# Performance work log

Measured on AMD Instinct MI355X. Metric: run time of the kernel, lower is better.

The kernel has to match this reference:

```python
import jax, jax.numpy as jnp
import numpy as np
from jax import lax

B, T, E, D, CC, K, H = 64, 2000, 512, 1024, 32, 31, 128
PAD = (K - 1) // 2


def setup_inputs() -> dict:
    key = jax.random.key(0)
    ks = jax.random.split(key, 12)
    enc_output = jax.random.normal(ks[0], (B, T, E), dtype=jnp.float32)
    text_len = jax.random.randint(ks[1], (B,), 1, T + 1)
    dec_state = jax.random.normal(ks[2], (B, D), dtype=jnp.float32)
    prev_att_w = jax.random.uniform(ks[3], (B, T), dtype=jnp.float32)
    # learned parameters
    W_enc = jax.random.normal(ks[4], (E, H), dtype=jnp.float32) / np.sqrt(E)
    b_enc = jnp.zeros((H,), dtype=jnp.float32)
    W_dec = jax.random.normal(ks[5], (D, H), dtype=jnp.float32) / np.sqrt(D)
    W_att = jax.random.normal(ks[6], (CC, H), dtype=jnp.float32) / np.sqrt(CC)
    conv_w = jax.random.normal(ks[7], (CC, 1, K), dtype=jnp.float32) / np.sqrt(K)  # OIH
    W_out = jax.random.normal(ks[8], (H, 1), dtype=jnp.float32) / np.sqrt(H)
    b_out = jnp.zeros((1,), dtype=jnp.float32)
    return {
        'enc_output': enc_output, 'text_len': text_len, 'dec_state': dec_state,
        'prev_att_w': prev_att_w, 'W_enc': W_enc, 'b_enc': b_enc, 'W_dec': W_dec,
        'W_att': W_att, 'conv_w': conv_w, 'W_out': W_out, 'b_out': b_out,
    }


def reference(enc_output, text_len, dec_state, prev_att_w,
              W_enc, b_enc, W_dec, W_att, conv_w, W_out, b_out):
    # processed_memory = fc_enc(enc_output): (B,T,H)
    pm = jnp.einsum('bte,eh->bth', enc_output, W_enc) + b_enc
    # location conv: (B,1,T) -> (B,CC,T), same padding, no bias
    att_conv = lax.conv_general_dilated(
        prev_att_w[:, None, :], conv_w, window_strides=(1,),
        padding=[(PAD, PAD)], dimension_numbers=('NCH', 'OIH', 'NCH'))
    # fc_att on channel dim: (B,T,H)
    att_conv = jnp.einsum('bct,ch->bth', att_conv, W_att)
    # fc_dec(dec_state): (B,1,H)
    dec = (dec_state @ W_dec)[:, None, :]
    # energy: (B,T)
    energy = (jnp.tanh(att_conv + pm + dec) @ W_out)[..., 0] + b_out[0]
    att_w = jax.nn.softmax(energy, axis=1)  # (B,T)
    att_c = jnp.einsum('bte,bt->be', enc_output, att_w)  # (B,E)
    return att_c, att_w
```

## Files before the change

### kernel.cpp

```cpp
#include <hip/hip_runtime.h>

typedef short bf16x8 __attribute__((ext_vector_type(8)));
typedef float f32x4 __attribute__((ext_vector_type(4)));


__device__ __forceinline__ unsigned short f2bf(float f) {
  unsigned int u = __builtin_bit_cast(unsigned int, f);
  u += 0x7fffu + ((u >> 16) & 1u);
  return (unsigned short)(u >> 16);
}

__global__ __launch_bounds__(128) void prep_dec_kernel(
    const float* __restrict__ dec_state, const float* __restrict__ W_dec,
    const float* __restrict__ b_enc, float* __restrict__ decb)
{
  const int b = blockIdx.x;
  const int h = threadIdx.x;
  __shared__ float sd[1024];
  for (int i = h; i < 1024; i += 128) sd[i] = dec_state[b*1024 + i];
  __syncthreads();
  float acc = b_enc[h];
  #pragma unroll 8
  for (int d = 0; d < 1024; ++d) acc = fmaf(sd[d], W_dec[d*128 + h], acc);
  decb[b*128 + h] = acc;
}

__global__ __launch_bounds__(256) void prep_misc_kernel(
    const float* __restrict__ conv_w, const float* __restrict__ W_att,
    const float* __restrict__ W_enc, float* __restrict__ Mkh,
    unsigned short* __restrict__ WT)
{
  if (blockIdx.x == 64) {
    const int h = threadIdx.x;
    if (h < 128) {
      for (int k = 0; k < 31; ++k) {
        float a = 0.f;
        #pragma unroll
        for (int c = 0; c < 32; ++c) a = fmaf(conv_w[c*31 + k], W_att[c*128 + h], a);
        Mkh[k*128 + h] = a;
      }
    }
  } else {
    const int e0 = blockIdx.x * 8;
    #pragma unroll
    for (int j = 0; j < 4; ++j) {
      int idx = threadIdx.x + j*256;
      int el = idx >> 7, h = idx & 127;
      int e = e0 + el;
      float v = W_enc[e*128 + h];
      WT[(e >> 6)*8192 + h*64 + (e & 63)] = f2bf(v);
    }
  }
}

__global__ __launch_bounds__(256) void energy_kernel(
    const float* __restrict__ enc, const float* __restrict__ prev,
    const unsigned short* __restrict__ WT, const float* __restrict__ Mkh,
    const float* __restrict__ decb, const float* __restrict__ W_out,
    float* __restrict__ energy)
{
  __shared__ __align__(16) unsigned short sA[64*64];
  __shared__ __align__(16) unsigned short sB[128*64];
  __shared__ float sM[31*128];
  __shared__ float sDecb[128];
  __shared__ float sWout[128];
  __shared__ float sPrev[96];

  const int b  = blockIdx.y;
  const int t0 = blockIdx.x * 64;
  const int tid = threadIdx.x;

  for (int i = tid; i < 31*128; i += 256) sM[i] = Mkh[i];
  if (tid < 128) { sDecb[tid] = decb[b*128 + tid]; sWout[tid] = W_out[tid]; }
  if (tid < 96) {
    int tt = t0 + tid - 15;
    sPrev[tid] = (tt >= 0 && tt < 2000) ? prev[b*2000 + tt] : 0.f;
  }

  f32x4 acc[8];
  #pragma unroll
  for (int i = 0; i < 8; ++i) acc[i] = (f32x4){0.f, 0.f, 0.f, 0.f};

  const int wave = tid >> 6, lane = tid & 63;
  const int lr = lane & 15, lg = lane >> 4;
  char* sAc = (char*)sA;
  char* sBc = (char*)sB;
  const int xorv = (lr & 7) << 4;
  const int rowA = (wave*16 + lr) * 128;

  const float* encB = enc + (size_t)b * (2000u*512u);
  const float* gsrc[4]; int dstA[4];
  #pragma unroll
  for (int i = 0; i < 4; ++i) {
    int s = tid + i*256;
    int tl = s >> 4, e4 = s & 15;
    int tg = t0 + tl; if (tg > 1999) tg = 1999;
    gsrc[i] = encB + (size_t)tg*512 + e4*4;
    dstA[i] = (tl*128 + e4*8) ^ ((tl & 7) << 4);
  }
  const int hB = tid >> 1, halfB = tid & 1;

  for (int kc = 0; kc < 8; ++kc) {
    #pragma unroll
    for (int i = 0; i < 4; ++i) {
      const float4 v = *reinterpret_cast<const float4*>(gsrc[i] + kc*64);
      uint2 w;
      w.x = ((unsigned)f2bf(v.y) << 16) | f2bf(v.x);
      w.y = ((unsigned)f2bf(v.w) << 16) | f2bf(v.z);
      *reinterpret_cast<uint2*>(sAc + dstA[i]) = w;
    }
    {
      const unsigned short* src = WT + kc*8192 + tid*32;
      #pragma unroll
      for (int q = 0; q < 4; ++q) {
        uint4 v = *reinterpret_cast<const uint4*>(src + q*8);
        *reinterpret_cast<uint4*>(sBc + ((hB*128 + halfB*64 + q*16) ^ ((hB & 7) << 4))) = v;
      }
    }
    __syncthreads();
    #pragma unroll
    for (int ks = 0; ks < 2; ++ks) {
      bf16x8 a = *reinterpret_cast<const bf16x8*>(sAc + ((rowA + ks*64 + lg*16) ^ xorv));
      #pragma unroll
      for (int nt = 0; nt < 8; ++nt) {
        bf16x8 bb = *reinterpret_cast<const bf16x8*>(
            sBc + (((nt*16 + lr)*128 + ks*64 + lg*16) ^ xorv));
        acc[nt] = __builtin_amdgcn_mfma_f32_16x16x32_bf16(a, bb, acc[nt], 0, 0, 0);
      }
    }
    __syncthreads();
  }

  const int tbase = wave*16 + lg*4;
  #pragma unroll 1
  for (int k = 0; k < 31; ++k) {
    float p0 = sPrev[tbase + 0 + k];
    float p1 = sPrev[tbase + 1 + k];
    float p2 = sPrev[tbase + 2 + k];
    float p3 = sPrev[tbase + 3 + k];
    const float* mrow = sM + k*128 + lr;
    #pragma unroll
    for (int nt = 0; nt < 8; ++nt) {
      float m = mrow[nt*16];
      acc[nt][0] = fmaf(p0, m, acc[nt][0]);
      acc[nt][1] = fmaf(p1, m, acc[nt][1]);
      acc[nt][2] = fmaf(p2, m, acc[nt][2]);
      acc[nt][3] = fmaf(p3, m, acc[nt][3]);
    }
  }

  float es0 = 0.f, es1 = 0.f, es2 = 0.f, es3 = 0.f;
  #pragma unroll
  for (int nt = 0; nt < 8; ++nt) {
    float dh = sDecb[nt*16 + lr];
    float wo = sWout[nt*16 + lr];
    es0 += tanhf(acc[nt][0] + dh) * wo;
    es1 += tanhf(acc[nt][1] + dh) * wo;
    es2 += tanhf(acc[nt][2] + dh) * wo;
    es3 += tanhf(acc[nt][3] + dh) * wo;
  }
  #pragma unroll
  for (int off = 1; off < 16; off <<= 1) {
    es0 += __shfl_xor(es0, off, 64);
    es1 += __shfl_xor(es1, off, 64);
    es2 += __shfl_xor(es2, off, 64);
    es3 += __shfl_xor(es3, off, 64);
  }
  if (lr == 0) {
    int t = t0 + tbase;
    float ev[4] = {es0, es1, es2, es3};
    #pragma unroll
    for (int r = 0; r < 4; ++r)
      if (t + r < 2000) energy[b*2000 + t + r] = ev[r];
  }
}

__global__ __launch_bounds__(256) void softmax_kernel(
    const float* __restrict__ energy, float* __restrict__ attw)
{
  const int b = blockIdx.x, tid = threadIdx.x;
  __shared__ float red[4];
  __shared__ float red2[4];
  float m = -1e30f;
  for (int i = tid; i < 2000; i += 256) m = fmaxf(m, energy[b*2000 + i]);
  #pragma unroll
  for (int off = 1; off < 64; off <<= 1) m = fmaxf(m, __shfl_xor(m, off, 64));
  if ((tid & 63) == 0) red[tid >> 6] = m;
  __syncthreads();
  m = fmaxf(fmaxf(red[0], red[1]), fmaxf(red[2], red[3]));

  float s = 0.f;
  for (int i = tid; i < 2000; i += 256) {
    float p = __expf(energy[b*2000 + i] - m);
    attw[b*2000 + i] = p;
    s += p;
  }
  #pragma unroll
  for (int off = 1; off < 64; off <<= 1) s += __shfl_xor(s, off, 64);
  if ((tid & 63) == 0) red2[tid >> 6] = s;
  __syncthreads();
  s = red2[0] + red2[1] + red2[2] + red2[3];
  float inv = 1.f / s;
  for (int i = tid; i < 2000; i += 256) attw[b*2000 + i] *= inv;
}

__global__ __launch_bounds__(256) void attc_partial_kernel(
    const float* __restrict__ enc, const float* __restrict__ attw,
    float* __restrict__ part)
{
  const int b = blockIdx.y, ch = blockIdx.x, tid = threadIdx.x;
  const int tstart = ch * 125, tend = tstart + 125;
  float a0 = 0.f, a1 = 0.f;
  const float2* e2 = reinterpret_cast<const float2*>(enc + (size_t)b * (2000u*512u));
  for (int t = tstart; t < tend; ++t) {
    float w = attw[b*2000 + t];
    float2 v = e2[t*256 + tid];
    a0 = fmaf(v.x, w, a0);
    a1 = fmaf(v.y, w, a1);
  }
  part[((b*16 + ch)*512) + tid*2 + 0] = a0;
  part[((b*16 + ch)*512) + tid*2 + 1] = a1;
}

__global__ __launch_bounds__(512) void attc_reduce_kernel(
    const float* __restrict__ part, float* __restrict__ out)
{
  const int b = blockIdx.x, e = threadIdx.x;
  float s = 0.f;
  #pragma unroll
  for (int c = 0; c < 16; ++c) s += part[(b*16 + c)*512 + e];
  out[b*512 + e] = s;
}

extern "C" void kernel_launch(void* const* d_in, const int* in_sizes, int n_in,
                              void* d_out, int out_size, void* d_ws, size_t ws_size,
                              hipStream_t stream) {
  (void)in_sizes; (void)n_in; (void)out_size; (void)ws_size;
  const float* enc       = (const float*)d_in[0];
  const float* dec_state = (const float*)d_in[2];
  const float* prev      = (const float*)d_in[3];
  const float* W_enc     = (const float*)d_in[4];
  const float* b_enc     = (const float*)d_in[5];
  const float* W_dec     = (const float*)d_in[6];
  const float* W_att     = (const float*)d_in[7];
  const float* conv_w    = (const float*)d_in[8];
  const float* W_out     = (const float*)d_in[9];

  char* ws = (char*)d_ws;
  float*          energy = (float*)(ws + 0);
  float*          decb   = (float*)(ws + 524288);
  float*          Mkh    = (float*)(ws + 557056);
  unsigned short* WT     = (unsigned short*)(ws + 573440);
  float*          part   = (float*)(ws + 704512);

  float* attc = (float*)d_out;
  float* attw = (float*)d_out + 64*512;

  prep_dec_kernel <<<64, 128, 0, stream>>>(dec_state, W_dec, b_enc, decb);
  prep_misc_kernel<<<65, 256, 0, stream>>>(conv_w, W_att, W_enc, Mkh, WT);
  energy_kernel   <<<dim3(32, 64), 256, 0, stream>>>(enc, prev, WT, Mkh, decb, W_out, energy);
  softmax_kernel  <<<64, 256, 0, stream>>>(energy, attw);
  attc_partial_kernel<<<dim3(16, 64), 256, 0, stream>>>(enc, attw, part);
  attc_reduce_kernel <<<64, 512, 0, stream>>>(part, attc);
}
```

Baseline: 190.7 us.

## Merge prep kernels, prefetch encoder tiles, switch to fp16 MFMA, vectorize attc

The two prep kernels are merged into one launch. The energy GEMM loop now loads the next encoder K-chunk into registers while the current chunk is being computed, and it uses fp16 MFMA instead of bf16. The attention-context partial kernel reads float4 with two time-parity groups per block, and the reduce kernel sums 32 vectorized partials. The aim is to hide global-load latency in the bandwidth-bound encoder passes and to cut launch overhead, at the cost of more registers and fp16 range limits on the encoder activations.

New measurement: 198.1 us. +3.9%, slower.

```diff
diff --git a/kernel.cpp b/kernel.cpp
--- a/kernel.cpp
+++ b/kernel.cpp
@@ -1,38 +1,45 @@
 #include <hip/hip_runtime.h>
-
-typedef short bf16x8 __attribute__((ext_vector_type(8)));
+#include <hip/hip_fp16.h>
+
+typedef _Float16 f16x8 __attribute__((ext_vector_type(8)));
 typedef float f32x4 __attribute__((ext_vector_type(4)));
 
 
-__device__ __forceinline__ unsigned short f2bf(float f) {
-  unsigned int u = __builtin_bit_cast(unsigned int, f);
-  u += 0x7fffu + ((u >> 16) & 1u);
-  return (unsigned short)(u >> 16);
-}
-
-__global__ __launch_bounds__(128) void prep_dec_kernel(
+__device__ __forceinline__ unsigned short f2h(float f) {
+  __half h = __float2half(f);
+  return __builtin_bit_cast(unsigned short, h);
+}
+
+__global__ __launch_bounds__(256) void prep_kernel(
     const float* __restrict__ dec_state, const float* __restrict__ W_dec,
-    const float* __restrict__ b_enc, float* __restrict__ decb)
-{
-  const int b = blockIdx.x;
-  const int h = threadIdx.x;
-  __shared__ float sd[1024];
-  for (int i = h; i < 1024; i += 128) sd[i] = dec_state[b*1024 + i];
-  __syncthreads();
-  float acc = b_enc[h];
-  #pragma unroll 8
-  for (int d = 0; d < 1024; ++d) acc = fmaf(sd[d], W_dec[d*128 + h], acc);
-  decb[b*128 + h] = acc;
-}
-
-__global__ __launch_bounds__(256) void prep_misc_kernel(
-    const float* __restrict__ conv_w, const float* __restrict__ W_att,
-    const float* __restrict__ W_enc, float* __restrict__ Mkh,
+    const float* __restrict__ b_enc, const float* __restrict__ conv_w,
+    const float* __restrict__ W_att, const float* __restrict__ W_enc,
+    float* __restrict__ decb, float* __restrict__ Mkh,
     unsigned short* __restrict__ WT)
 {
-  if (blockIdx.x == 64) {
-    const int h = threadIdx.x;
-    if (h < 128) {
+  const int blk = blockIdx.x, tid = threadIdx.x;
+  if (blk < 32) {
+    __shared__ float sd[2048];
+    const int sub = tid >> 7, h = tid & 127;
+    const int b = blk*2 + sub;
+    for (int i = h; i < 1024; i += 128) sd[sub*1024 + i] = dec_state[b*1024 + i];
+    __syncthreads();
+    float acc = b_enc[h];
+    #pragma unroll 8
+    for (int d = 0; d < 1024; ++d) acc = fmaf(sd[sub*1024 + d], W_dec[d*128 + h], acc);
+    decb[b*128 + h] = acc;
+  } else if (blk < 96) {
+    const int e0 = (blk - 32) * 8;
+    #pragma unroll
+    for (int j = 0; j < 4; ++j) {
+      int idx = tid + j*256;
+      int el = idx >> 7, hh = idx & 127;
+      int e = e0 + el;
+      WT[(e >> 6)*8192 + hh*64 + (e & 63)] = f2h(W_enc[e*128 + hh]);
+    }
+  } else {
+    if (tid < 128) {
+      const int h = tid;
       for (int k = 0; k < 31; ++k) {
         float a = 0.f;
         #pragma unroll
@@ -40,16 +47,6 @@
         Mkh[k*128 + h] = a;
       }
     }
-  } else {
-    const int e0 = blockIdx.x * 8;
-    #pragma unroll
-    for (int j = 0; j < 4; ++j) {
-      int idx = threadIdx.x + j*256;
-      int el = idx >> 7, h = idx & 127;
-      int e = e0 + el;
-      float v = W_enc[e*128 + h];
-      WT[(e >> 6)*8192 + h*64 + (e & 63)] = f2bf(v);
-    }
   }
 }
 
@@ -99,36 +96,49 @@
     dstA[i] = (tl*128 + e4*8) ^ ((tl & 7) << 4);
   }
   const int hB = tid >> 1, halfB = tid & 1;
+  const int swB = (hB & 7) << 4;
+
+  float4 ra[4];
+  #pragma unroll
+  for (int i = 0; i < 4; ++i) ra[i] = *reinterpret_cast<const float4*>(gsrc[i]);
 
   for (int kc = 0; kc < 8; ++kc) {
+    uint4 rb[4];
+    const unsigned short* srcB = WT + kc*8192 + tid*32;
+    #pragma unroll
+    for (int q = 0; q < 4; ++q) rb[q] = reinterpret_cast<const uint4*>(srcB)[q];
+    float4 na[4];
+    if (kc < 7) {
+      #pragma unroll
+      for (int i = 0; i < 4; ++i)
+        na[i] = *reinterpret_cast<const float4*>(gsrc[i] + (kc+1)*64);
+    }
     #pragma unroll
     for (int i = 0; i < 4; ++i) {
-      const float4 v = *reinterpret_cast<const float4*>(gsrc[i] + kc*64);
       uint2 w;
-      w.x = ((unsigned)f2bf(v.y) << 16) | f2bf(v.x);
-      w.y = ((unsigned)f2bf(v.w) << 16) | f2bf(v.z);
+      w.x = ((unsigned)f2h(ra[i].y) << 16) | f2h(ra[i].x);
+      w.y = ((unsigned)f2h(ra[i].w) << 16) | f2h(ra[i].z);
       *reinterpret_cast<uint2*>(sAc + dstA[i]) = w;
     }
-    {
-      const unsigned short* src = WT + kc*8192 + tid*32;
-      #pragma unroll
-      for (int q = 0; q < 4; ++q) {
-        uint4 v = *reinterpret_cast<const uint4*>(src + q*8);
-        *reinterpret_cast<uint4*>(sBc + ((hB*128 + halfB*64 + q*16) ^ ((hB & 7) << 4))) = v;
-      }
-    }
+    #pragma unroll
+    for (int q = 0; q < 4; ++q)
+      *reinterpret_cast<uint4*>(sBc + ((hB*128 + halfB*64 + q*16) ^ swB)) = rb[q];
     __syncthreads();
     #pragma unroll
     for (int ks = 0; ks < 2; ++ks) {
-      bf16x8 a = *reinterpret_cast<const bf16x8*>(sAc + ((rowA + ks*64 + lg*16) ^ xorv));
+      f16x8 a = *reinterpret_cast<const f16x8*>(sAc + ((rowA + ks*64 + lg*16) ^ xorv));
       #pragma unroll
       for (int nt = 0; nt < 8; ++nt) {
-        bf16x8 bb = *reinterpret_cast<const bf16x8*>(
+        f16x8 bb = *reinterpret_cast<const f16x8*>(
             sBc + (((nt*16 + lr)*128 + ks*64 + lg*16) ^ xorv));
-        acc[nt] = __builtin_amdgcn_mfma_f32_16x16x32_bf16(a, bb, acc[nt], 0, 0, 0);
+        acc[nt] = __builtin_amdgcn_mfma_f32_16x16x32_f16(a, bb, acc[nt], 0, 0, 0);
       }
     }
     __syncthreads();
+    if (kc < 7) {
+      #pragma unroll
+      for (int i = 0; i < 4; ++i) ra[i] = na[i];
+    }
   }
 
   const int tbase = wave*16 + lg*4;
@@ -209,27 +219,35 @@
     float* __restrict__ part)
 {
   const int b = blockIdx.y, ch = blockIdx.x, tid = threadIdx.x;
-  const int tstart = ch * 125, tend = tstart + 125;
-  float a0 = 0.f, a1 = 0.f;
-  const float2* e2 = reinterpret_cast<const float2*>(enc + (size_t)b * (2000u*512u));
-  for (int t = tstart; t < tend; ++t) {
+  const int p = tid >> 7;
+  const int e4 = (tid & 127) * 4;
+  const int tstart = ch * 125 + p, tend = ch * 125 + 125;
+  const float* encB = enc + (size_t)b * (2000u*512u);
+  float a0 = 0.f, a1 = 0.f, a2 = 0.f, a3 = 0.f;
+  #pragma unroll 2
+  for (int t = tstart; t < tend; t += 2) {
     float w = attw[b*2000 + t];
-    float2 v = e2[t*256 + tid];
+    float4 v = *reinterpret_cast<const float4*>(encB + (size_t)t*512 + e4);
     a0 = fmaf(v.x, w, a0);
     a1 = fmaf(v.y, w, a1);
-  }
-  part[((b*16 + ch)*512) + tid*2 + 0] = a0;
-  part[((b*16 + ch)*512) + tid*2 + 1] = a1;
-}
-
-__global__ __launch_bounds__(512) void attc_reduce_kernel(
+    a2 = fmaf(v.z, w, a2);
+    a3 = fmaf(v.w, w, a3);
+  }
+  float4 out = {a0, a1, a2, a3};
+  *reinterpret_cast<float4*>(part + ((size_t)(b*32 + ch*2 + p))*512 + e4) = out;
+}
+
+__global__ __launch_bounds__(128) void attc_reduce_kernel(
     const float* __restrict__ part, float* __restrict__ out)
 {
-  const int b = blockIdx.x, e = threadIdx.x;
-  float s = 0.f;
-  #pragma unroll
-  for (int c = 0; c < 16; ++c) s += part[(b*16 + c)*512 + e];
-  out[b*512 + e] = s;
+  const int b = blockIdx.x, e4 = threadIdx.x * 4;
+  float4 s = {0.f, 0.f, 0.f, 0.f};
+  #pragma unroll
+  for (int c = 0; c < 32; ++c) {
+    float4 v = *reinterpret_cast<const float4*>(part + ((size_t)(b*32 + c))*512 + e4);
+    s.x += v.x; s.y += v.y; s.z += v.z; s.w += v.w;
+  }
+  *reinterpret_cast<float4*>(out + b*512 + e4) = s;
 }
 
 extern "C" void kernel_launch(void* const* d_in, const int* in_sizes, int n_in,
@@ -256,10 +274,10 @@
   float* attc = (float*)d_out;
   float* attw = (float*)d_out + 64*512;
 
-  prep_dec_kernel <<<64, 128, 0, stream>>>(dec_state, W_dec, b_enc, decb);
-  prep_misc_kernel<<<65, 256, 0, stream>>>(conv_w, W_att, W_enc, Mkh, WT);
-  energy_kernel   <<<dim3(32, 64), 256, 0, stream>>>(enc, prev, WT, Mkh, decb, W_out, energy);
-  softmax_kernel  <<<64, 256, 0, stream>>>(energy, attw);
+  prep_kernel        <<<97, 256, 0, stream>>>(dec_state, W_dec, b_enc, conv_w, W_att, W_enc,
+                                              decb, Mkh, WT);
+  energy_kernel      <<<dim3(32, 64), 256, 0, stream>>>(enc, prev, WT, Mkh, decb, W_out, energy);
+  softmax_kernel     <<<64, 256, 0, stream>>>(energy, attw);
   attc_partial_kernel<<<dim3(16, 64), 256, 0, stream>>>(enc, attw, part);
-  attc_reduce_kernel <<<64, 512, 0, stream>>>(part, attc);
-}
+  attc_reduce_kernel <<<64, 128, 0, stream>>>(part, attc);
+}
```
